# Optimization experiments

Hardware: AMD Instinct MI355X
Metric: run time of the kernel (lower is better)

The kernel has to match this reference:

```python
import jax, jax.numpy as jnp
import numpy as np

N = 100000
E = 3200000

def spmm(edge_row, edge_col, edge_val, support):
    # out[i] = sum_{(i,j) in edges} w_ij * support[j]
    gathered = support[edge_col] * edge_val[:, None]  # [E, F]
    return jax.ops.segment_sum(gathered, edge_row, num_segments=N)

def setup_inputs() -> dict:
    key = jax.random.key(0)
    ks = jax.random.split(key, 10)
    x = jax.random.normal(ks[0], (N, 512), dtype=jnp.float32)
    edge_row = jax.random.randint(ks[1], (E,), 0, N, dtype=jnp.int32)
    edge_col = jax.random.randint(ks[2], (E,), 0, N, dtype=jnp.int32)
    edge_val = jax.random.uniform(ks[3], (E,), dtype=jnp.float32) / 32.0  # ~normalized adj
    def glorot_like(k, shape):
        stdv = 1.0 / np.sqrt(shape[-1])
        return jax.random.uniform(k, shape, dtype=jnp.float32, minval=-stdv, maxval=stdv)
    W1 = glorot_like(ks[4], (512, 256)); b1 = glorot_like(ks[5], (256,))
    W2 = glorot_like(ks[6], (256, 256)); b2 = glorot_like(ks[7], (256,))
    W3 = glorot_like(ks[8], (256, 64)); b3 = glorot_like(ks[9], (64,))
    return {"x": x, "edge_row": edge_row, "edge_col": edge_col, "edge_val": edge_val,
            "W1": W1, "b1": b1, "W2": W2, "b2": b2, "W3": W3, "b3": b3}

def reference(x, edge_row, edge_col, edge_val, W1, b1, W2, b2, W3, b3):
    # layer 1: mm + spmm + bias + relu
    h = spmm(edge_row, edge_col, edge_val, x @ W1) + b1
    h = jax.nn.relu(h)
    # hidden layer (layer_num=3 -> one hidden GraphConvolution); dropout is inference no-op
    h = spmm(edge_row, edge_col, edge_val, h @ W2) + b2
    h = jax.nn.relu(h)
    # output layer
    h = spmm(edge_row, edge_col, edge_val, h @ W3) + b3
    # task='nodecls', ppi=False
    return jax.nn.log_softmax(h, axis=1)
```

## Files before the change

kernel.cpp:

```cpp
#include <hip/hip_runtime.h>
#include <stdint.h>
#include <stddef.h>

typedef __bf16 bf16x8 __attribute__((ext_vector_type(8)));
typedef float  f32x4  __attribute__((ext_vector_type(4)));
typedef float  f32x2  __attribute__((ext_vector_type(2)));

static __device__ __forceinline__ float bf2f(unsigned short u) {
    union { unsigned int i; float f; } v; v.i = ((unsigned int)u) << 16; return v.f;
}
static __device__ __forceinline__ unsigned short f2bf(float f) {
    union { float f; unsigned int i; } v; v.f = f;
    unsigned int r = v.i + 0x7FFFu + ((v.i >> 16) & 1u);
    return (unsigned short)(r >> 16);
}
static __device__ __forceinline__ unsigned char f2fp8(float f) {
    return (unsigned char)(__builtin_amdgcn_cvt_pk_fp8_f32(f, f, 0, false) & 0xFF);
}

#define N_NODES 100000
#define N_EDGES 3200000
#define MPAD    100096
#define NB      782
#define NBLK    256
#define EB      (N_EDGES / NBLK)
#define COLMASK 0xFFFFF


__global__ __launch_bounds__(256) void bucket_hist(const int* __restrict__ er, int* __restrict__ blockCnt) {
    __shared__ int h[NB];
    for (int i = threadIdx.x; i < NB; i += 256) h[i] = 0;
    __syncthreads();
    int base = blockIdx.x * EB;
    for (int e = base + threadIdx.x; e < base + EB; e += 256)
        atomicAdd(&h[er[e] >> 7], 1);
    __syncthreads();
    for (int i = threadIdx.x; i < NB; i += 256) blockCnt[blockIdx.x * NB + i] = h[i];
}

__global__ __launch_bounds__(256) void bucket_scan_a(const int* __restrict__ blockCnt,
                                                     int* __restrict__ blockOff,
                                                     int* __restrict__ bucketTotal) {
    __shared__ int s[256];
    int b = blockIdx.x, t = threadIdx.x;
    int v = blockCnt[t * NB + b];
    s[t] = v; __syncthreads();
    for (int off = 1; off < 256; off <<= 1) {
        int u = (t >= off) ? s[t - off] : 0;
        __syncthreads();
        s[t] += u;
        __syncthreads();
    }
    blockOff[t * NB + b] = s[t] - v;
    if (t == 255) bucketTotal[b] = s[255];
}

__global__ __launch_bounds__(1024) void bucket_scan_b(const int* __restrict__ bucketTotal,
                                                      int* __restrict__ bucketStart,
                                                      int* __restrict__ rp, int E) {
    __shared__ int s[1024];
    int t = threadIdx.x;
    int v = (t < NB) ? bucketTotal[t] : 0;
    s[t] = v; __syncthreads();
    for (int off = 1; off < 1024; off <<= 1) {
        int u = (t >= off) ? s[t - off] : 0;
        __syncthreads();
        s[t] += u;
        __syncthreads();
    }
    if (t < NB) bucketStart[t] = s[t] - v;
    if (t == 0) { bucketStart[NB] = E; rp[N_NODES] = E; }
}

__global__ __launch_bounds__(256) void bucket_scatter(const int* __restrict__ er, const int* __restrict__ ec,
                                                      const float* __restrict__ ev,
                                                      const int* __restrict__ blockOff,
                                                      const int* __restrict__ bucketStart,
                                                      int2* __restrict__ cpackT) {
    __shared__ int cur[NB];
    for (int i = threadIdx.x; i < NB; i += 256)
        cur[i] = bucketStart[i] + blockOff[blockIdx.x * NB + i];
    __syncthreads();
    int base = blockIdx.x * EB;
    for (int e = base + threadIdx.x; e < base + EB; e += 256) {
        int r = er[e];
        int p = atomicAdd(&cur[r >> 7], 1);
        cpackT[p] = make_int2(((r & 127) << 20) | ec[e], __float_as_int(ev[e]));
    }
}

__global__ __launch_bounds__(256) void bucket_sort(const int2* __restrict__ cpackT,
                                                   const int* __restrict__ bucketStart,
                                                   int2* __restrict__ cpack, int* __restrict__ rp) {
    __shared__ int cnt[128];
    __shared__ int cursor[128];
    int b = blockIdx.x, t = threadIdx.x;
    int s = bucketStart[b], e = bucketStart[b + 1];
    if (t < 128) cnt[t] = 0;
    __syncthreads();
    for (int j = s + t; j < e; j += 256)
        atomicAdd(&cnt[cpackT[j].x >> 20], 1);
    __syncthreads();
    int val = (t < 128) ? cnt[t] : 0;
    for (int off = 1; off < 128; off <<= 1) {
        int u = (t < 128 && t >= off) ? cnt[t - off] : 0;
        __syncthreads();
        if (t < 128) cnt[t] += u;
        __syncthreads();
    }
    if (t < 128) {
        int excl = cnt[t] - val;
        cursor[t] = s + excl;
        int gr = b * 128 + t;
        if (gr < N_NODES) rp[gr] = s + excl;
    }
    __syncthreads();
    for (int j = s + t; j < e; j += 256) {
        int2 v = cpackT[j];
        int p = atomicAdd(&cursor[v.x >> 20], 1);
        cpack[p] = v;
    }
}

__global__ __launch_bounds__(256) void transpose_all(const float* __restrict__ W1, unsigned short* __restrict__ Wt1,
                                                     const float* __restrict__ W2, unsigned short* __restrict__ Wt2,
                                                     const float* __restrict__ W3, unsigned short* __restrict__ Wt3) {
    int i = blockIdx.x * 256 + threadIdx.x;
    const int S1 = 512 * 256, S2 = 256 * 256, S3 = 256 * 64;
    if (i < S1) {
        int k = i / 256, n = i % 256;
        Wt1[(size_t)n * 512 + k] = f2bf(W1[i]);
    } else if (i < S1 + S2) {
        int j = i - S1; int k = j / 256, n = j % 256;
        Wt2[(size_t)n * 256 + k] = f2bf(W2[j]);
    } else if (i < S1 + S2 + S3) {
        int j = i - S1 - S2; int k = j / 64, n = j % 64;
        Wt3[(size_t)n * 256 + k] = f2bf(W3[j]);
    }
}

template<int BM, int BN, int BK, bool A_F32, int OUT>
__global__ __launch_bounds__(256) void gemm_mfma(const void* __restrict__ Aptr,
                                                 const unsigned short* __restrict__ Bt,
                                                 void* __restrict__ Cptr,
                                                 int K, int Nc, int Mclamp) {
    constexpr int WROWS = 2, WCOLS = 2;
    constexpr int WM = BM / WROWS, WN = BN / WCOLS;
    constexpr int MT = WM / 16, NT = WN / 16;
    constexpr int LDA = BK + 8;
    constexpr int KV = BK / 8;

    __shared__ unsigned short lds_a[BM * LDA];
    __shared__ unsigned short lds_b[BN * LDA];

    const int tid  = threadIdx.x;
    const int wid  = tid >> 6, lane = tid & 63;
    const int wrow = wid >> 1, wcol = wid & 1;
    const int bm = blockIdx.x * BM, bn = blockIdx.y * BN;
    const int r = lane & 15, q = lane >> 4;

    const float*          Af = (const float*)Aptr;
    const unsigned short* Ab = (const unsigned short*)Aptr;

    f32x4 acc[MT][NT];
    f32x4 zero = {0.f, 0.f, 0.f, 0.f};
#pragma unroll
    for (int mi = 0; mi < MT; mi++)
#pragma unroll
        for (int ni = 0; ni < NT; ni++) acc[mi][ni] = zero;

    for (int k0 = 0; k0 < K; k0 += BK) {
#pragma unroll
        for (int it = 0; it < (BM * KV) / 256; it++) {
            int v = tid + it * 256;
            int row = v / KV, kc = (v % KV) * 8;
            int grow = bm + row;
            uint4 d;
            if constexpr (A_F32) {
                grow = (grow <= Mclamp) ? grow : Mclamp;
                const float4* pp = (const float4*)(Af + (size_t)grow * K + k0 + kc);
                float4 f0 = pp[0], f1 = pp[1];
                d.x = (unsigned)f2bf(f0.x) | ((unsigned)f2bf(f0.y) << 16);
                d.y = (unsigned)f2bf(f0.z) | ((unsigned)f2bf(f0.w) << 16);
                d.z = (unsigned)f2bf(f1.x) | ((unsigned)f2bf(f1.y) << 16);
                d.w = (unsigned)f2bf(f1.z) | ((unsigned)f2bf(f1.w) << 16);
            } else {
                d = *(const uint4*)(Ab + (size_t)grow * K + k0 + kc);
            }
            *(uint4*)&lds_a[row * LDA + kc] = d;
        }
#pragma unroll
        for (int it = 0; it < (BN * KV) / 256; it++) {
            int v = tid + it * 256;
            int row = v / KV, kc = (v % KV) * 8;
            uint4 d = *(const uint4*)(Bt + (size_t)(bn + row) * K + k0 + kc);
            *(uint4*)&lds_b[row * LDA + kc] = d;
        }
        __syncthreads();

#pragma unroll
        for (int kk = 0; kk < BK; kk += 32) {
            bf16x8 av[MT], bv[NT];
#pragma unroll
            for (int mi = 0; mi < MT; mi++)
                av[mi] = *(const bf16x8*)&lds_a[(wrow * WM + mi * 16 + r) * LDA + kk + q * 8];
#pragma unroll
            for (int ni = 0; ni < NT; ni++)
                bv[ni] = *(const bf16x8*)&lds_b[(wcol * WN + ni * 16 + r) * LDA + kk + q * 8];
#pragma unroll
            for (int mi = 0; mi < MT; mi++)
#pragma unroll
                for (int ni = 0; ni < NT; ni++)
                    acc[mi][ni] = __builtin_amdgcn_mfma_f32_16x16x32_bf16(av[mi], bv[ni], acc[mi][ni], 0, 0, 0);
        }
        __syncthreads();
    }

#pragma unroll
    for (int mi = 0; mi < MT; mi++) {
        int row = bm + wrow * WM + mi * 16 + q * 4;
#pragma unroll
        for (int ni = 0; ni < NT; ni++) {
            int cc = bn + wcol * WN + ni * 16 + r;
#pragma unroll
            for (int d = 0; d < 4; d++) {
                if constexpr (OUT == 0) {
                    ((unsigned short*)Cptr)[(size_t)(row + d) * Nc + cc] = f2bf(acc[mi][ni][d]);
                } else {
                    ((unsigned char*)Cptr)[(size_t)(row + d) * Nc + cc] = f2fp8(acc[mi][ni][d]);
                }
            }
        }
    }
}

__global__ __launch_bounds__(256) void spmm_f256_fp8(const int* __restrict__ rp, const int2* __restrict__ cpack,
                                                     const unsigned char* __restrict__ Z8,
                                                     const float* __restrict__ bias, unsigned short* __restrict__ H, int N) {
    int w = (blockIdx.x * 256 + threadIdx.x) >> 6;
    if (w >= N) return;
    int lane = threadIdx.x & 63;
    int f4 = lane * 4;
    int s = rp[w], e = rp[w + 1];
    float a0 = 0.f, a1 = 0.f, a2 = 0.f, a3 = 0.f;
    int j = s;
    for (; j + 8 <= e; j += 8) {
        const int4* ep = (const int4*)(cpack + j);
        int4 p0 = ep[0], p1 = ep[1], p2 = ep[2], p3 = ep[3];
        unsigned z0 = *(const unsigned*)(Z8 + (size_t)(p0.x & COLMASK) * 256 + f4);
        unsigned z1 = *(const unsigned*)(Z8 + (size_t)(p0.z & COLMASK) * 256 + f4);
        unsigned z2 = *(const unsigned*)(Z8 + (size_t)(p1.x & COLMASK) * 256 + f4);
        unsigned z3 = *(const unsigned*)(Z8 + (size_t)(p1.z & COLMASK) * 256 + f4);
        unsigned z4 = *(const unsigned*)(Z8 + (size_t)(p2.x & COLMASK) * 256 + f4);
        unsigned z5 = *(const unsigned*)(Z8 + (size_t)(p2.z & COLMASK) * 256 + f4);
        unsigned z6 = *(const unsigned*)(Z8 + (size_t)(p3.x & COLMASK) * 256 + f4);
        unsigned z7 = *(const unsigned*)(Z8 + (size_t)(p3.z & COLMASK) * 256 + f4);
        float w0 = __int_as_float(p0.y), w1 = __int_as_float(p0.w);
        float w2 = __int_as_float(p1.y), w3 = __int_as_float(p1.w);
        float w4 = __int_as_float(p2.y), w5 = __int_as_float(p2.w);
        float w6 = __int_as_float(p3.y), w7 = __int_as_float(p3.w);
#define ACC8(Z, W) { \
        f32x2 lo = __builtin_amdgcn_cvt_pk_f32_fp8((int)(Z), false); \
        f32x2 hi = __builtin_amdgcn_cvt_pk_f32_fp8((int)(Z), true);  \
        a0 += (W) * lo.x; a1 += (W) * lo.y; a2 += (W) * hi.x; a3 += (W) * hi.y; }
        ACC8(z0, w0) ACC8(z1, w1) ACC8(z2, w2) ACC8(z3, w3)
        ACC8(z4, w4) ACC8(z5, w5) ACC8(z6, w6) ACC8(z7, w7)
    }
    if (j < e) {
#pragma unroll
        for (int t = 0; t < 8; t++) {
            int jj = j + t;
            int2 ed = (jj < e) ? cpack[jj] : make_int2(0, 0);
            float wt = __int_as_float(ed.y);
            unsigned z = *(const unsigned*)(Z8 + (size_t)(ed.x & COLMASK) * 256 + f4);
            ACC8(z, wt)
        }
    }
#undef ACC8
    float4 b = *(const float4*)(bias + f4);
    a0 = fmaxf(a0 + b.x, 0.f); a1 = fmaxf(a1 + b.y, 0.f);
    a2 = fmaxf(a2 + b.z, 0.f); a3 = fmaxf(a3 + b.w, 0.f);
    ushort4 o; o.x = f2bf(a0); o.y = f2bf(a1); o.z = f2bf(a2); o.w = f2bf(a3);
    *(ushort4*)(H + (size_t)w * 256 + f4) = o;
}

__global__ __launch_bounds__(256) void spmm_f64_lsm(const int* __restrict__ rp, const int2* __restrict__ cpack,
                                                    const unsigned short* __restrict__ Z,
                                                    const float* __restrict__ bias, float* __restrict__ out, int N) {
    int w = (blockIdx.x * 256 + threadIdx.x) >> 6;
    if (w >= N) return;
    int lane = threadIdx.x & 63;
    int g = lane >> 4, fl = lane & 15;
    int s = rp[w], e = rp[w + 1];
    float a0 = 0.f, a1 = 0.f, a2 = 0.f, a3 = 0.f;
    for (int j = s; j < e; j += 8) {
        int j0 = j + g, j1 = j + 4 + g;
        int2 e0 = (j0 < e) ? cpack[j0] : make_int2(0, 0);
        int2 e1 = (j1 < e) ? cpack[j1] : make_int2(0, 0);
        ushort4 z0 = *(const ushort4*)(Z + (size_t)(e0.x & COLMASK) * 64 + fl * 4);
        ushort4 z1 = *(const ushort4*)(Z + (size_t)(e1.x & COLMASK) * 64 + fl * 4);
        float w0 = __int_as_float(e0.y), w1 = __int_as_float(e1.y);
        a0 += w0 * bf2f(z0.x); a1 += w0 * bf2f(z0.y); a2 += w0 * bf2f(z0.z); a3 += w0 * bf2f(z0.w);
        a0 += w1 * bf2f(z1.x); a1 += w1 * bf2f(z1.y); a2 += w1 * bf2f(z1.z); a3 += w1 * bf2f(z1.w);
    }
    a0 += __shfl_xor(a0, 16, 64); a1 += __shfl_xor(a1, 16, 64);
    a2 += __shfl_xor(a2, 16, 64); a3 += __shfl_xor(a3, 16, 64);
    a0 += __shfl_xor(a0, 32, 64); a1 += __shfl_xor(a1, 32, 64);
    a2 += __shfl_xor(a2, 32, 64); a3 += __shfl_xor(a3, 32, 64);
    float4 b = *(const float4*)(bias + fl * 4);
    a0 += b.x; a1 += b.y; a2 += b.z; a3 += b.w;
    float m = fmaxf(fmaxf(a0, a1), fmaxf(a2, a3));
    for (int off = 1; off <= 8; off <<= 1) m = fmaxf(m, __shfl_xor(m, off, 64));
    float sum = __expf(a0 - m) + __expf(a1 - m) + __expf(a2 - m) + __expf(a3 - m);
    for (int off = 1; off <= 8; off <<= 1) sum += __shfl_xor(sum, off, 64);
    float lse = m + __logf(sum);
    if (g == 0) {
        float4 o = make_float4(a0 - lse, a1 - lse, a2 - lse, a3 - lse);
        *(float4*)(out + (size_t)w * 64 + fl * 4) = o;
    }
}

extern "C" void kernel_launch(void* const* d_in, const int* in_sizes, int n_in,
                              void* d_out, int out_size, void* d_ws, size_t ws_size,
                              hipStream_t stream) {
    const float* x  = (const float*)d_in[0];
    const int*   er = (const int*)  d_in[1];
    const int*   ec = (const int*)  d_in[2];
    const float* ev = (const float*)d_in[3];
    const float* W1 = (const float*)d_in[4];
    const float* b1 = (const float*)d_in[5];
    const float* W2 = (const float*)d_in[6];
    const float* b2 = (const float*)d_in[7];
    const float* W3 = (const float*)d_in[8];
    const float* b3 = (const float*)d_in[9];

    const int N = N_NODES, E = N_EDGES;

    char* p = (char*)d_ws;
    auto alloc = [&](size_t bytes) -> char* {
        char* q = p; p += (bytes + 255) & ~(size_t)255; return q;
    };
    unsigned short* Wt1    = (unsigned short*)alloc((size_t)256 * 512 * 2);
    unsigned short* Wt2    = (unsigned short*)alloc((size_t)256 * 256 * 2);
    unsigned short* Wt3    = (unsigned short*)alloc((size_t)64  * 256 * 2);
    int*            rp     = (int*)  alloc((size_t)(N + 1) * 4);
    int*            blkCnt = (int*)  alloc((size_t)NBLK * NB * 4);
    int*            blkOff = (int*)  alloc((size_t)NBLK * NB * 4);
    int*            bktTot = (int*)  alloc((size_t)NB * 4);
    int*            bktSt  = (int*)  alloc((size_t)(NB + 1) * 4);
    int2*           cpack  = (int2*) alloc((size_t)E * 8);
    unsigned char*  Z8     = (unsigned char*) alloc((size_t)MPAD * 256);
    unsigned short* bufA   = (unsigned short*)alloc((size_t)MPAD * 256 * 2);
    unsigned short* bufB   = (unsigned short*)alloc((size_t)MPAD * 256 * 2);
    int2*           cpackT = (int2*)bufA;

    bucket_hist   <<<NBLK, 256, 0, stream>>>(er, blkCnt);
    bucket_scan_a <<<NB,   256, 0, stream>>>(blkCnt, blkOff, bktTot);
    bucket_scan_b <<<1,   1024, 0, stream>>>(bktTot, bktSt, rp, E);
    bucket_scatter<<<NBLK, 256, 0, stream>>>(er, ec, ev, blkOff, bktSt, cpackT);
    bucket_sort   <<<NB,   256, 0, stream>>>(cpackT, bktSt, cpack, rp);

    transpose_all<<<(512*256 + 256*256 + 256*64 + 255) / 256, 256, 0, stream>>>(W1, Wt1, W2, Wt2, W3, Wt3);

    gemm_mfma<64, 256, 64, true , 1><<<dim3(MPAD / 64, 1), 256, 0, stream>>>(x,    Wt1, Z8,   512, 256, N - 1);
    spmm_f256_fp8<<<N / 4, 256, 0, stream>>>(rp, cpack, Z8, b1, bufB, N);
    gemm_mfma<64, 256, 64, false, 1><<<dim3(MPAD / 64, 1), 256, 0, stream>>>(bufB, Wt2, Z8,   256, 256, N - 1);
    spmm_f256_fp8<<<N / 4, 256, 0, stream>>>(rp, cpack, Z8, b2, bufB, N);
    gemm_mfma<128, 64, 64, false, 0><<<dim3(MPAD / 128, 1), 256, 0, stream>>>(bufB, Wt3, bufA, 256, 64, N - 1);
    spmm_f64_lsm<<<N / 4, 256, 0, stream>>>(rp, cpack, bufA, b3, (float*)d_out, N);
}
```

Baseline: 830.9 us.

## Use scalar edge loads and prescaled byte offsets in SpMM kernels

Edge records are rewritten during the bucket sort to hold the column already shifted to a byte offset into the fp8 feature table. The SpMM kernels now read edge entries as wave-uniform scalars through readfirstlane, so each lane no longer loads and masks the index itself. The inner loop is unrolled to 16 with a masked tail that relies on zero padding past the end of the edge array. The final 64-wide layer is reorganized so each lane owns one feature, replacing the four-group partial sums and cross-group shuffles with a single full-wave softmax reduction. The risk is that the scalar loads may not be scheduled well and that the per-edge serial gather may reduce memory-level parallelism.

```diff
diff --git a/kernel.cpp b/kernel.cpp
--- a/kernel.cpp
+++ b/kernel.cpp
@@ -57,7 +57,8 @@
 
 __global__ __launch_bounds__(1024) void bucket_scan_b(const int* __restrict__ bucketTotal,
                                                       int* __restrict__ bucketStart,
-                                                      int* __restrict__ rp, int E) {
+                                                      int* __restrict__ rp, int E,
+                                                      int2* __restrict__ cpad) {
     __shared__ int s[1024];
     int t = threadIdx.x;
     int v = (t < NB) ? bucketTotal[t] : 0;
@@ -69,7 +70,10 @@
         __syncthreads();
     }
     if (t < NB) bucketStart[t] = s[t] - v;
-    if (t == 0) { bucketStart[NB] = E; rp[N_NODES] = E; }
+    if (t == 0) {
+        bucketStart[NB] = E; rp[N_NODES] = E;
+        for (int i = 0; i < 16; i++) cpad[i] = make_int2(0, 0);
+    }
 }
 
 __global__ __launch_bounds__(256) void bucket_scatter(const int* __restrict__ er, const int* __restrict__ ec,
@@ -118,7 +122,7 @@
     for (int j = s + t; j < e; j += 256) {
         int2 v = cpackT[j];
         int p = atomicAdd(&cursor[v.x >> 20], 1);
-        cpack[p] = v;
+        cpack[p] = make_int2((v.x & COLMASK) << 8, v.y);
     }
 }
 
@@ -237,49 +241,40 @@
 __global__ __launch_bounds__(256) void spmm_f256_fp8(const int* __restrict__ rp, const int2* __restrict__ cpack,
                                                      const unsigned char* __restrict__ Z8,
                                                      const float* __restrict__ bias, unsigned short* __restrict__ H, int N) {
-    int w = (blockIdx.x * 256 + threadIdx.x) >> 6;
+    int w = __builtin_amdgcn_readfirstlane((int)((blockIdx.x * 256 + threadIdx.x) >> 6));
     if (w >= N) return;
     int lane = threadIdx.x & 63;
     int f4 = lane * 4;
-    int s = rp[w], e = rp[w + 1];
-    float a0 = 0.f, a1 = 0.f, a2 = 0.f, a3 = 0.f;
+    int s = __builtin_amdgcn_readfirstlane(rp[w]);
+    int e = __builtin_amdgcn_readfirstlane(rp[w + 1]);
+    f32x2 acc01 = {0.f, 0.f}, acc23 = {0.f, 0.f};
     int j = s;
-    for (; j + 8 <= e; j += 8) {
-        const int4* ep = (const int4*)(cpack + j);
-        int4 p0 = ep[0], p1 = ep[1], p2 = ep[2], p3 = ep[3];
-        unsigned z0 = *(const unsigned*)(Z8 + (size_t)(p0.x & COLMASK) * 256 + f4);
-        unsigned z1 = *(const unsigned*)(Z8 + (size_t)(p0.z & COLMASK) * 256 + f4);
-        unsigned z2 = *(const unsigned*)(Z8 + (size_t)(p1.x & COLMASK) * 256 + f4);
-        unsigned z3 = *(const unsigned*)(Z8 + (size_t)(p1.z & COLMASK) * 256 + f4);
-        unsigned z4 = *(const unsigned*)(Z8 + (size_t)(p2.x & COLMASK) * 256 + f4);
-        unsigned z5 = *(const unsigned*)(Z8 + (size_t)(p2.z & COLMASK) * 256 + f4);
-        unsigned z6 = *(const unsigned*)(Z8 + (size_t)(p3.x & COLMASK) * 256 + f4);
-        unsigned z7 = *(const unsigned*)(Z8 + (size_t)(p3.z & COLMASK) * 256 + f4);
-        float w0 = __int_as_float(p0.y), w1 = __int_as_float(p0.w);
-        float w2 = __int_as_float(p1.y), w3 = __int_as_float(p1.w);
-        float w4 = __int_as_float(p2.y), w5 = __int_as_float(p2.w);
-        float w6 = __int_as_float(p3.y), w7 = __int_as_float(p3.w);
-#define ACC8(Z, W) { \
-        f32x2 lo = __builtin_amdgcn_cvt_pk_f32_fp8((int)(Z), false); \
-        f32x2 hi = __builtin_amdgcn_cvt_pk_f32_fp8((int)(Z), true);  \
-        a0 += (W) * lo.x; a1 += (W) * lo.y; a2 += (W) * hi.x; a3 += (W) * hi.y; }
-        ACC8(z0, w0) ACC8(z1, w1) ACC8(z2, w2) ACC8(z3, w3)
-        ACC8(z4, w4) ACC8(z5, w5) ACC8(z6, w6) ACC8(z7, w7)
-    }
-    if (j < e) {
-#pragma unroll
-        for (int t = 0; t < 8; t++) {
-            int jj = j + t;
-            int2 ed = (jj < e) ? cpack[jj] : make_int2(0, 0);
-            float wt = __int_as_float(ed.y);
-            unsigned z = *(const unsigned*)(Z8 + (size_t)(ed.x & COLMASK) * 256 + f4);
-            ACC8(z, wt)
-        }
-    }
-#undef ACC8
+
+#define EDGE_BLK(UN, MASKED) { \
+        int2 eb[UN]; \
+        _Pragma("unroll") \
+        for (int t = 0; t < UN; t++) eb[t] = cpack[j + t]; \
+        _Pragma("unroll") \
+        for (int t = 0; t < UN; t++) { \
+            int ex = __builtin_amdgcn_readfirstlane(eb[t].x); \
+            int ew = __builtin_amdgcn_readfirstlane(eb[t].y); \
+            if (MASKED) ew = (j + t < e) ? ew : 0; \
+            float wt = __int_as_float(ew); \
+            unsigned z = *(const unsigned*)(Z8 + (size_t)(unsigned)ex + f4); \
+            f32x2 lo = __builtin_amdgcn_cvt_pk_f32_fp8((int)z, false); \
+            f32x2 hi = __builtin_amdgcn_cvt_pk_f32_fp8((int)z, true);  \
+            f32x2 wv = {wt, wt}; \
+            acc01 += wv * lo; \
+            acc23 += wv * hi; \
+        } }
+
+    for (; j + 16 <= e; j += 16) EDGE_BLK(16, false)
+    for (; j < e; j += 8)        EDGE_BLK(8,  true)
+#undef EDGE_BLK
+
     float4 b = *(const float4*)(bias + f4);
-    a0 = fmaxf(a0 + b.x, 0.f); a1 = fmaxf(a1 + b.y, 0.f);
-    a2 = fmaxf(a2 + b.z, 0.f); a3 = fmaxf(a3 + b.w, 0.f);
+    float a0 = fmaxf(acc01.x + b.x, 0.f), a1 = fmaxf(acc01.y + b.y, 0.f);
+    float a2 = fmaxf(acc23.x + b.z, 0.f), a3 = fmaxf(acc23.y + b.w, 0.f);
     ushort4 o; o.x = f2bf(a0); o.y = f2bf(a1); o.z = f2bf(a2); o.w = f2bf(a3);
     *(ushort4*)(H + (size_t)w * 256 + f4) = o;
 }
@@ -287,37 +282,43 @@
 __global__ __launch_bounds__(256) void spmm_f64_lsm(const int* __restrict__ rp, const int2* __restrict__ cpack,
                                                     const unsigned short* __restrict__ Z,
                                                     const float* __restrict__ bias, float* __restrict__ out, int N) {
-    int w = (blockIdx.x * 256 + threadIdx.x) >> 6;
+    int w = __builtin_amdgcn_readfirstlane((int)((blockIdx.x * 256 + threadIdx.x) >> 6));
     if (w >= N) return;
     int lane = threadIdx.x & 63;
-    int g = lane >> 4, fl = lane & 15;
-    int s = rp[w], e = rp[w + 1];
-    float a0 = 0.f, a1 = 0.f, a2 = 0.f, a3 = 0.f;
-    for (int j = s; j < e; j += 8) {
-        int j0 = j + g, j1 = j + 4 + g;
-        int2 e0 = (j0 < e) ? cpack[j0] : make_int2(0, 0);
-        int2 e1 = (j1 < e) ? cpack[j1] : make_int2(0, 0);
-        ushort4 z0 = *(const ushort4*)(Z + (size_t)(e0.x & COLMASK) * 64 + fl * 4);
-        ushort4 z1 = *(const ushort4*)(Z + (size_t)(e1.x & COLMASK) * 64 + fl * 4);
-        float w0 = __int_as_float(e0.y), w1 = __int_as_float(e1.y);
-        a0 += w0 * bf2f(z0.x); a1 += w0 * bf2f(z0.y); a2 += w0 * bf2f(z0.z); a3 += w0 * bf2f(z0.w);
-        a0 += w1 * bf2f(z1.x); a1 += w1 * bf2f(z1.y); a2 += w1 * bf2f(z1.z); a3 += w1 * bf2f(z1.w);
-    }
-    a0 += __shfl_xor(a0, 16, 64); a1 += __shfl_xor(a1, 16, 64);
-    a2 += __shfl_xor(a2, 16, 64); a3 += __shfl_xor(a3, 16, 64);
-    a0 += __shfl_xor(a0, 32, 64); a1 += __shfl_xor(a1, 32, 64);
-    a2 += __shfl_xor(a2, 32, 64); a3 += __shfl_xor(a3, 32, 64);
-    float4 b = *(const float4*)(bias + fl * 4);
-    a0 += b.x; a1 += b.y; a2 += b.z; a3 += b.w;
-    float m = fmaxf(fmaxf(a0, a1), fmaxf(a2, a3));
-    for (int off = 1; off <= 8; off <<= 1) m = fmaxf(m, __shfl_xor(m, off, 64));
-    float sum = __expf(a0 - m) + __expf(a1 - m) + __expf(a2 - m) + __expf(a3 - m);
-    for (int off = 1; off <= 8; off <<= 1) sum += __shfl_xor(sum, off, 64);
-    float lse = m + __logf(sum);
-    if (g == 0) {
-        float4 o = make_float4(a0 - lse, a1 - lse, a2 - lse, a3 - lse);
-        *(float4*)(out + (size_t)w * 64 + fl * 4) = o;
-    }
+    const unsigned char* Zb = (const unsigned char*)Z;
+    int s = __builtin_amdgcn_readfirstlane(rp[w]);
+    int e = __builtin_amdgcn_readfirstlane(rp[w + 1]);
+    float acc = 0.f;
+    int j = s;
+
+#define EDGE_BLK(UN, MASKED) { \
+        int2 eb[UN]; \
+        _Pragma("unroll") \
+        for (int t = 0; t < UN; t++) eb[t] = cpack[j + t]; \
+        _Pragma("unroll") \
+        for (int t = 0; t < UN; t++) { \
+            int ex = __builtin_amdgcn_readfirstlane(eb[t].x); \
+            int ew = __builtin_amdgcn_readfirstlane(eb[t].y); \
+            if (MASKED) ew = (j + t < e) ? ew : 0; \
+            float wt = __int_as_float(ew); \
+             \
+            unsigned short z = *(const unsigned short*)(Zb + (size_t)(unsigned)(ex >> 1) + lane * 2); \
+            acc += wt * bf2f(z); \
+        } }
+
+    for (; j + 8 <= e; j += 8) EDGE_BLK(8, false)
+    for (; j < e; j += 4)      EDGE_BLK(4, true)
+#undef EDGE_BLK
+
+    float a = acc + bias[lane];
+    float m = a;
+#pragma unroll
+    for (int off = 32; off >= 1; off >>= 1) m = fmaxf(m, __shfl_xor(m, off, 64));
+    float p = __expf(a - m);
+    float sum = p;
+#pragma unroll
+    for (int off = 32; off >= 1; off >>= 1) sum += __shfl_xor(sum, off, 64);
+    out[(size_t)w * 64 + lane] = a - m - __logf(sum);
 }
 
 extern "C" void kernel_launch(void* const* d_in, const int* in_sizes, int n_in,
@@ -348,7 +349,7 @@
     int*            blkOff = (int*)  alloc((size_t)NBLK * NB * 4);
     int*            bktTot = (int*)  alloc((size_t)NB * 4);
     int*            bktSt  = (int*)  alloc((size_t)(NB + 1) * 4);
-    int2*           cpack  = (int2*) alloc((size_t)E * 8);
+    int2*           cpack  = (int2*) alloc((size_t)(E + 16) * 8);
     unsigned char*  Z8     = (unsigned char*) alloc((size_t)MPAD * 256);
     unsigned short* bufA   = (unsigned short*)alloc((size_t)MPAD * 256 * 2);
     unsigned short* bufB   = (unsigned short*)alloc((size_t)MPAD * 256 * 2);
@@ -356,7 +357,7 @@
 
     bucket_hist   <<<NBLK, 256, 0, stream>>>(er, blkCnt);
     bucket_scan_a <<<NB,   256, 0, stream>>>(blkCnt, blkOff, bktTot);
-    bucket_scan_b <<<1,   1024, 0, stream>>>(bktTot, bktSt, rp, E);
+    bucket_scan_b <<<1,   1024, 0, stream>>>(bktTot, bktSt, rp, E, cpack + E);
     bucket_scatter<<<NBLK, 256, 0, stream>>>(er, ec, ev, blkOff, bktSt, cpackT);
     bucket_sort   <<<NB,   256, 0, stream>>>(cpackT, bktSt, cpack, rp);
 
```

After: 815.7 us. About the same (-1.8%).
